# Optimization experiments

Measured on AMD Instinct MI355X. Metric: run time of the kernel, lower is better.

Reference implementation:

```python
import jax, jax.numpy as jnp
import numpy as np

F = 256   # nb_features
H = 8     # nb_heads
B = 4
S = 1024  # q_s == kv_s
SCALE = F ** 0.5  # module MULTIPLIES scores by sqrt(f) when scale=True


def setup_inputs() -> dict:
    key = jax.random.key(0)
    ks = jax.random.split(key, 6)
    return {
        "q_input": jax.random.normal(ks[0], (B, F, S), dtype=jnp.float32),
        "kv_input": jax.random.normal(ks[1], (B, F, S), dtype=jnp.float32),
        "Wq": jax.random.normal(ks[2], (F, F * H), dtype=jnp.float32) * (F ** -0.5),
        "Wk": jax.random.normal(ks[3], (F, F * H), dtype=jnp.float32) * (F ** -0.5),
        "Wv": jax.random.normal(ks[4], (F, F * H), dtype=jnp.float32) * (F ** -0.5),
        "Wz": jax.random.normal(ks[5], (F * H, F), dtype=jnp.float32) * ((F * H) ** -0.5),
    }


def reference(q_input, kv_input, Wq, Wk, Wv, Wz):
    b, f, q_s = q_input.shape
    kv_s = kv_input.shape[2]
    h = H
    # (b, f, s) -> (b, s, f)
    qx = jnp.transpose(q_input, (0, 2, 1))
    kvx = jnp.transpose(kv_input, (0, 2, 1))
    # Linear f -> f*h, then split last dim into (f, h)
    q = (qx @ Wq).reshape(b, q_s, f, h)
    k = (kvx @ Wk).reshape(b, kv_s, f, h)
    v = (kvx @ Wv).reshape(b, kv_s, f, h)
    # sigmoid-gated attention: scores MULTIPLIED by sqrt(f)
    qkt = jnp.einsum('bifh,bjfh->bijh', q, k)
    attn = jax.nn.sigmoid(qkt * SCALE)
    weighted_v = jnp.einsum('bijh,bjfh->bifh', attn, v)  # (b, q_s, f, h)
    z = weighted_v.reshape(b * q_s, f * h)
    out = jax.nn.relu(z @ Wz)  # dropout p=0.0 -> identity
    return jnp.transpose(out.reshape(b, q_s, f), (0, 2, 1))  # (b, f, q_s)
```

## Files before the change

### kernel.cpp

```cpp
#include <hip/hip_runtime.h>
#include <hip/hip_fp16.h>

typedef _Float16 f16;
typedef _Float16 f16x8 __attribute__((ext_vector_type(8)));
typedef float f32x4 __attribute__((ext_vector_type(4)));
typedef unsigned u32x4 __attribute__((ext_vector_type(4)));

#define AS1(p) ((const __attribute__((address_space(1))) void*)(p))
#define AS3(p) ((__attribute__((address_space(3))) void*)(p))

__device__ __forceinline__ void gload16(const void* g, void* l) {
  __builtin_amdgcn_global_load_lds(AS1(g), AS3(l), 16, 0, 0);
}

__device__ __forceinline__ float sgm(float x) {
  return __builtin_amdgcn_rcpf(1.0f + __builtin_amdgcn_exp2f(x * -23.083120654223414f));
}

__device__ __forceinline__ void tbody(const float* __restrict__ ip,
                                      f16* __restrict__ op,
                                      long in_rs, long out_rs) {
  __shared__ float t[64][68];
  int tid = threadIdx.x;
  {
    int c4 = (tid & 15) * 4, r0 = tid >> 4;
#pragma unroll
    for (int p = 0; p < 4; ++p) {
      int r = r0 + 16 * p;
      float4 v = *(const float4*)(ip + (long)r * in_rs + c4);
      t[c4 + 0][r] = v.x; t[c4 + 1][r] = v.y; t[c4 + 2][r] = v.z; t[c4 + 3][r] = v.w;
    }
  }
  __syncthreads();
  {
    int r4 = (tid & 15) * 4, c0 = tid >> 4;
#pragma unroll
    for (int p = 0; p < 4; ++p) {
      int c = c0 + 16 * p;
      float4 v = *(const float4*)(&t[c][r4]);
      union { f16 h[4]; unsigned long long u; } pk;
      pk.h[0] = (f16)v.x; pk.h[1] = (f16)v.y; pk.h[2] = (f16)v.z; pk.h[3] = (f16)v.w;
      *(unsigned long long*)(op + (long)c * out_rs + r4) = pk.u;
    }
  }
}

__global__ __launch_bounds__(256) void tall(
    const float* __restrict__ qin, const float* __restrict__ kvin,
    const float* __restrict__ Wq, const float* __restrict__ Wk,
    const float* __restrict__ Wv, const float* __restrict__ Wz,
    f16* __restrict__ Xq, f16* __restrict__ Xkv,
    f16* __restrict__ Wqt, f16* __restrict__ Wkt, f16* __restrict__ Wvt,
    f16* __restrict__ Wzt) {
  int id = blockIdx.x;
  if (id < 512) {
    int x = id & 15, y = (id >> 4) & 3, z = id >> 6;
    const float* in = (z < 4) ? qin : kvin;
    f16* out = (z < 4) ? Xq : Xkv;
    long b = z & 3;
    tbody(in + b * 262144 + (long)(y * 64) * 1024 + x * 64,
          out + b * 262144 + (long)(x * 64) * 256 + y * 64, 1024, 256);
  } else if (id < 896) {
    int t = id - 512;
    int x = t & 31, y = (t >> 5) & 3, z = t >> 7;
    const float* in = (z == 0) ? Wq : (z == 1) ? Wk : Wv;
    f16* out = (z == 0) ? Wqt : (z == 1) ? Wkt : Wvt;
    tbody(in + (long)(y * 64) * 2048 + x * 64,
          out + (long)(x * 64) * 256 + y * 64, 2048, 256);
  } else {
    int t = id - 896;
    int x = t & 3, y = (t >> 2) & 3;
    long z = t >> 4;
    tbody(Wz + z * 256 + (long)(y * 64) * 2048 + x * 64,
          Wzt + z * 256 + (long)(x * 64) * 2048 + y * 64, 2048, 2048);
  }
}

__global__ __launch_bounds__(256) void projk(
    const f16* __restrict__ Xq, const f16* __restrict__ Xkv,
    const f16* __restrict__ Wqt, const f16* __restrict__ Wkt, const f16* __restrict__ Wvt,
    f16* __restrict__ Qh, f16* __restrict__ Kh, f16* __restrict__ Vt) {
  __shared__ char sm[65536];
  int z = blockIdx.z;
  const f16* A = (z == 0) ? Xq : Xkv;
  const f16* B = (z == 0) ? Wqt : (z == 1) ? Wkt : Wvt;
  int m0 = blockIdx.x * 128, n0 = blockIdx.y * 128;
  int tid = threadIdx.x, wave = tid >> 6, lane = tid & 63;
  int wm = wave & 1, wn = wave >> 1;
  f32x4 acc[4][4];
#pragma unroll
  for (int i = 0; i < 4; ++i)
#pragma unroll
    for (int j = 0; j < 4; ++j) acc[i][j] = (f32x4){0.f, 0.f, 0.f, 0.f};

  auto PSTAGE = [&](int buf, int kt) {
    char* As = sm + buf * 32768;
    char* Bs = As + 16384;
    int k0 = kt * 64;
#pragma unroll
    for (int is = 0; is < 4; ++is) {
      int loff = is * 4096 + wave * 1024;
      int g = loff + lane * 16;
      int row = g >> 7, sl = (g >> 4) & 7;
      int sp = (sl ^ (row & 7)) * 8;
      gload16(A + (long)(m0 + row) * 256 + k0 + sp, As + loff);
      gload16(B + (long)(n0 + row) * 256 + k0 + sp, Bs + loff);
    }
  };

  PSTAGE(0, 0);
  __syncthreads();
  for (int kt = 0; kt < 4; ++kt) {
    int cur = kt & 1;
    if (kt < 3) PSTAGE(cur ^ 1, kt + 1);
    const char* As = sm + cur * 32768;
    const char* Bs = As + 16384;
#pragma unroll
    for (int t = 0; t < 2; ++t) {
      f16x8 af[4], bf[4];
#pragma unroll
      for (int mi = 0; mi < 4; ++mi) {
        int row = wm * 64 + mi * 16 + (lane & 15);
        int sl = (t * 4 + (lane >> 4)) ^ (row & 7);
        af[mi] = *(const f16x8*)(As + row * 128 + sl * 16);
      }
#pragma unroll
      for (int ni = 0; ni < 4; ++ni) {
        int row = wn * 64 + ni * 16 + (lane & 15);
        int sl = (t * 4 + (lane >> 4)) ^ (row & 7);
        bf[ni] = *(const f16x8*)(Bs + row * 128 + sl * 16);
      }
#pragma unroll
      for (int mi = 0; mi < 4; ++mi)
#pragma unroll
        for (int ni = 0; ni < 4; ++ni)
          acc[mi][ni] = __builtin_amdgcn_mfma_f32_16x16x32_f16(af[mi], bf[ni], acc[mi][ni], 0, 0, 0);
    }
    __syncthreads();
  }
#pragma unroll
  for (int mi = 0; mi < 4; ++mi)
#pragma unroll
    for (int ni = 0; ni < 4; ++ni) {
      int cc = wn * 64 + ni * 16 + (lane & 15);
      int rs0 = wm * 64 + mi * 16 + (lane >> 4) * 4;
      union { f16 h[4]; unsigned long long u; } pk;
#pragma unroll
      for (int r = 0; r < 4; ++r) pk.h[r] = (f16)acc[mi][ni][r];
      *(unsigned long long*)(sm + cc * 272 + rs0 * 2) = pk.u;
    }
  __syncthreads();
  if (z < 2) {
    f16* outp = (z == 0) ? Qh : Kh;
#pragma unroll
    for (int pass = 0; pass < 4; ++pass) {
      int item = pass * 256 + tid;
      int rs = item & 127, h = item >> 7;
      int m = m0 + rs, b = m >> 10, s = m & 1023;
      union { unsigned short u16[16]; uint4 q[2]; } pk;
#pragma unroll
      for (int u = 0; u < 16; ++u)
        pk.u16[u] = *(const unsigned short*)(sm + (h + 8 * u) * 272 + rs * 2);
      f16* dst = outp + ((long)(b * 8 + h) * 1024 + s) * 256 + (n0 >> 3);
      *(uint4*)dst = pk.q[0];
      *(uint4*)(dst + 8) = pk.q[1];
    }
  } else {
    int cc = tid >> 1, half = tid & 1;
    int c = n0 + cc, h = c & 7, fi = c >> 3;
    int m = m0 + half * 64;
    int b = m >> 10, s0 = m & 1023;
    uint4 q[8];
#pragma unroll
    for (int j = 0; j < 8; ++j)
      q[j] = *(const uint4*)(sm + cc * 272 + half * 128 + j * 16);
    f16* dst = Vt + ((long)(b * 8 + h) * 256 + fi) * 1024 + s0;
#pragma unroll
    for (int j = 0; j < 8; ++j) *(uint4*)(dst + j * 8) = q[j];
  }
}

__global__ __launch_bounds__(256) void attnk(
    const f16* __restrict__ Qh, const f16* __restrict__ Kh,
    const f16* __restrict__ Vt, f16* __restrict__ Zb) {
  __shared__ char sm[65536];
  int flat = blockIdx.x;
  int xcd = flat & 7, slotb = flat >> 3;
  int bh = xcd + 8 * (slotb & 3);
  int i0 = (slotb >> 2) * 64;
  int tid = threadIdx.x, wave = tid >> 6, lane = tid & 63;
  int l15 = lane & 15, l4 = lane >> 4;
  const f16* Qp = Qh + (long)bh * 262144;
  f16x8 q[8];
  {
    const f16* qr = Qp + (long)(i0 + wave * 16 + l15) * 256 + l4 * 8;
#pragma unroll
    for (int t = 0; t < 8; ++t) q[t] = *(const f16x8*)(qr + t * 32);
  }
  f32x4 acc[16];
#pragma unroll
  for (int n = 0; n < 16; ++n) acc[n] = (f32x4){0.f, 0.f, 0.f, 0.f};

  const char* kp[4];
  const char* vp[4];
  {
    const char* Kb = (const char*)(Kh + (long)bh * 262144);
    const char* Vb = (const char*)(Vt + (long)bh * 262144);
#pragma unroll
    for (int is = 0; is < 4; ++is) {
      int g = is * 4096 + wave * 1024 + lane * 16;
      int krow = g >> 9, ksl = (g >> 4) & 31;
      kp[is] = Kb + krow * 512 + ((ksl ^ krow) * 16);
      int f = g >> 6, jc = (g >> 4) & 3;
      vp[is] = Vb + f * 2048 + ((jc ^ ((f >> 1) & 3)) * 16);
    }
  }
  const int KB  = l15 * 512 + ((l4 * 16) ^ (l15 * 16));
  const int KB2 = KB + 8448;
  const int VB  = 16384 + l15 * 64 + ((l4 ^ ((l15 >> 1) & 3)) * 16);
  const int sdo = wave * 1024;

  auto STAGE = [&](int ob) {
#pragma unroll
    for (int is = 0; is < 4; ++is) {
      gload16(kp[is], sm + ob + is * 4096 + sdo);
      gload16(vp[is], sm + ob + 16384 + is * 4096 + sdo);
      kp[is] += 16384;
      vp[is] += 64;
    }
  };

  STAGE(0);
  __syncthreads();
  int bb = 0;
  for (int jt = 0; jt < 32; ++jt) {
    if (jt < 31) STAGE(bb ^ 32768);
    const int kb = KB ^ bb, kb2 = KB2 ^ bb, vb = VB ^ bb;
    f32x4 s0 = (f32x4){0.f, 0.f, 0.f, 0.f};
    f32x4 s1 = (f32x4){0.f, 0.f, 0.f, 0.f};
    __builtin_amdgcn_s_setprio(1);
#pragma unroll
    for (int t = 0; t < 8; ++t) {
      f16x8 k0 = *(const f16x8*)(sm + (kb ^ (t * 64)));
      f16x8 k1 = *(const f16x8*)(sm + (kb2 ^ (t * 64)));
      s0 = __builtin_amdgcn_mfma_f32_16x16x32_f16(k0, q[t], s0, 0, 0, 0);
      s1 = __builtin_amdgcn_mfma_f32_16x16x32_f16(k1, q[t], s1, 0, 0, 0);
    }
    __builtin_amdgcn_s_setprio(0);
    unsigned u00 = __builtin_bit_cast(unsigned, __builtin_amdgcn_cvt_pkrtz(sgm(s0[0]), sgm(s0[1])));
    unsigned u01 = __builtin_bit_cast(unsigned, __builtin_amdgcn_cvt_pkrtz(sgm(s0[2]), sgm(s0[3])));
    unsigned u10 = __builtin_bit_cast(unsigned, __builtin_amdgcn_cvt_pkrtz(sgm(s1[0]), sgm(s1[1])));
    unsigned u11 = __builtin_bit_cast(unsigned, __builtin_amdgcn_cvt_pkrtz(sgm(s1[2]), sgm(s1[3])));
    auto a0 = __builtin_amdgcn_permlane32_swap(u00, u10, false, false);
    auto w02 = __builtin_amdgcn_permlane16_swap(a0[0], a0[1], false, false);
    auto a1 = __builtin_amdgcn_permlane32_swap(u01, u11, false, false);
    auto w13 = __builtin_amdgcn_permlane16_swap(a1[0], a1[1], false, false);
    u32x4 paw;
    paw[0] = w02[0]; paw[1] = w13[0]; paw[2] = w02[1]; paw[3] = w13[1];
    f16x8 pav = __builtin_bit_cast(f16x8, paw);
    __builtin_amdgcn_s_setprio(1);
#pragma unroll
    for (int n = 0; n < 16; ++n) {
      f16x8 vbf = *(const f16x8*)(sm + (vb ^ (n * 1024)));
      acc[n] = __builtin_amdgcn_mfma_f32_16x16x32_f16(pav, vbf, acc[n], 0, 0, 0);
    }
    __builtin_amdgcn_s_setprio(0);
    __syncthreads();
    bb ^= 32768;
  }
#pragma unroll
  for (int nf = 0; nf < 16; ++nf)
#pragma unroll
    for (int r = 0; r < 4; ++r) {
      int il = wave * 16 + l4 * 4 + r;
      int f = nf * 16 + l15;
      *(f16*)(sm + il * 512 + ((f * 2) ^ (((il >> 2) & 3) << 5))) = (f16)acc[nf][r];
    }
  __syncthreads();
  f16* zp = Zb + ((long)bh * 1024 + i0) * 256;
#pragma unroll
  for (int c = 0; c < 8; ++c) {
    int il = c * 8 + (tid >> 5);
    int fb = (tid & 31) * 16;
    uint4 v = *(const uint4*)(sm + il * 512 + (fb ^ (((il >> 2) & 3) << 5)));
    *(uint4*)((char*)zp + il * 512 + fb) = v;
  }
}

__global__ __launch_bounds__(256) void zkern(
    const f16* __restrict__ Wzt, const f16* __restrict__ Zb,
    float* __restrict__ out) {
  __shared__ char sm[65536];
  int fo0 = blockIdx.x * 64, s0 = blockIdx.y * 64, b = blockIdx.z;
  int tid = threadIdx.x, wave = tid >> 6, lane = tid & 63;
  int wm = wave & 1, wn = wave >> 1;
  f32x4 acc[2][2];
#pragma unroll
  for (int i = 0; i < 2; ++i)
#pragma unroll
    for (int j = 0; j < 2; ++j) acc[i][j] = (f32x4){0.f, 0.f, 0.f, 0.f};

  auto ZSTAGE = [&](int buf, int kt) {
    char* As = sm + buf * 32768;
    char* Bs = As + 16384;
    int k0 = kt * 128, h = k0 >> 8, fi0 = k0 & 255;
#pragma unroll
    for (int is = 0; is < 4; ++is) {
      int loff = is * 4096 + wave * 1024;
      int g = loff + lane * 16;
      int row = g >> 8, sl = (g >> 4) & 15;
      int sp = (sl ^ (row & 15)) * 8;
      gload16(Wzt + (long)(fo0 + row) * 2048 + k0 + sp, As + loff);
      gload16(Zb + ((long)(b * 8 + h) * 1024 + s0 + row) * 256 + fi0 + sp, Bs + loff);
    }
  };

  ZSTAGE(0, 0);
  __syncthreads();
  for (int kt = 0; kt < 16; ++kt) {
    int cur = kt & 1;
    if (kt < 15) ZSTAGE(cur ^ 1, kt + 1);
    const char* As = sm + cur * 32768;
    const char* Bs = As + 16384;
#pragma unroll
    for (int t = 0; t < 4; ++t) {
      f16x8 af[2], bf[2];
#pragma unroll
      for (int mi = 0; mi < 2; ++mi) {
        int row = wm * 32 + mi * 16 + (lane & 15);
        int sl = (t * 4 + (lane >> 4)) ^ (row & 15);
        af[mi] = *(const f16x8*)(As + row * 256 + sl * 16);
      }
#pragma unroll
      for (int ni = 0; ni < 2; ++ni) {
        int row = wn * 32 + ni * 16 + (lane & 15);
        int sl = (t * 4 + (lane >> 4)) ^ (row & 15);
        bf[ni] = *(const f16x8*)(Bs + row * 256 + sl * 16);
      }
#pragma unroll
      for (int mi = 0; mi < 2; ++mi)
#pragma unroll
        for (int ni = 0; ni < 2; ++ni)
          acc[mi][ni] = __builtin_amdgcn_mfma_f32_16x16x32_f16(af[mi], bf[ni], acc[mi][ni], 0, 0, 0);
    }
    __syncthreads();
  }
#pragma unroll
  for (int mi = 0; mi < 2; ++mi)
#pragma unroll
    for (int ni = 0; ni < 2; ++ni)
#pragma unroll
      for (int r = 0; r < 4; ++r) {
        int fo = fo0 + wm * 32 + mi * 16 + (lane >> 4) * 4 + r;
        int s = s0 + wn * 32 + ni * 16 + (lane & 15);
        float v = acc[mi][ni][r];
        out[((long)b * 256 + fo) * 1024 + s] = v > 0.f ? v : 0.f;
      }
}

extern "C" void kernel_launch(void* const* d_in, const int* in_sizes, int n_in,
                              void* d_out, int out_size, void* d_ws, size_t ws_size,
                              hipStream_t stream) {
  const float* qin = (const float*)d_in[0];
  const float* kvin = (const float*)d_in[1];
  const float* Wq = (const float*)d_in[2];
  const float* Wk = (const float*)d_in[3];
  const float* Wv = (const float*)d_in[4];
  const float* Wz = (const float*)d_in[5];
  float* out = (float*)d_out;
  char* ws = (char*)d_ws;
  const long MB = 1 << 20;
  f16* Xq  = (f16*)(ws + 0 * MB);
  f16* Xkv = (f16*)(ws + 2 * MB);
  f16* Wqt = (f16*)(ws + 4 * MB);
  f16* Wkt = (f16*)(ws + 5 * MB);
  f16* Wvt = (f16*)(ws + 6 * MB);
  f16* Wzt = (f16*)(ws + 7 * MB);
  f16* Qh  = (f16*)(ws + 8 * MB);
  f16* Kh  = (f16*)(ws + 24 * MB);
  f16* Vt  = (f16*)(ws + 40 * MB);
  f16* Zb  = Qh;
  dim3 blk(256);
  tall<<<dim3(1024), blk, 0, stream>>>(qin, kvin, Wq, Wk, Wv, Wz,
                                       Xq, Xkv, Wqt, Wkt, Wvt, Wzt);
  projk<<<dim3(32, 16, 3), blk, 0, stream>>>(Xq, Xkv, Wqt, Wkt, Wvt, Qh, Kh, Vt);
  attnk<<<dim3(512), blk, 0, stream>>>(Qh, Kh, Vt, Zb);
  zkern<<<dim3(4, 16, 4), blk, 0, stream>>>(Wzt, Zb, out);
}
```

Before: 113.1 us.

## Switch attention kernel to 32x32x16 MFMA with two 32-row waves per block

The attention kernel moves from 4 waves of 16 query rows using 16x16x32 MFMA to 2 waves of 32 query rows using 32x32x16 MFMA, with a 128-thread block. Each wave now reads K and V tiles from LDS for twice as many rows, which cuts LDS traffic per FLOP, and sigmoid packing uses fewer lane permutes. The LDS-staged coalesced output store is replaced by direct scattered 2-byte global stores. Risks include lower occupancy from fewer waves per block, higher register use (16 q fragments and 8 f32x16 accumulators), and uncoalesced output writes.

```diff
diff --git a/kernel.cpp b/kernel.cpp
--- a/kernel.cpp
+++ b/kernel.cpp
@@ -4,6 +4,7 @@
 typedef _Float16 f16;
 typedef _Float16 f16x8 __attribute__((ext_vector_type(8)));
 typedef float f32x4 __attribute__((ext_vector_type(4)));
+typedef float f32x16 __attribute__((ext_vector_type(16)));
 typedef unsigned u32x4 __attribute__((ext_vector_type(4)));
 
 #define AS1(p) ((const __attribute__((address_space(1))) void*)(p))
@@ -15,6 +16,10 @@
 
 __device__ __forceinline__ float sgm(float x) {
   return __builtin_amdgcn_rcpf(1.0f + __builtin_amdgcn_exp2f(x * -23.083120654223414f));
+}
+
+__device__ __forceinline__ unsigned pk2(float a, float b) {
+  return __builtin_bit_cast(unsigned, __builtin_amdgcn_cvt_pkrtz(a, b));
 }
 
 __device__ __forceinline__ void tbody(const float* __restrict__ ip,
@@ -180,7 +185,7 @@
   }
 }
 
-__global__ __launch_bounds__(256) void attnk(
+__global__ __launch_bounds__(128) void attnk(
     const f16* __restrict__ Qh, const f16* __restrict__ Kh,
     const f16* __restrict__ Vt, f16* __restrict__ Zb) {
   __shared__ char sm[65536];
@@ -189,102 +194,90 @@
   int bh = xcd + 8 * (slotb & 3);
   int i0 = (slotb >> 2) * 64;
   int tid = threadIdx.x, wave = tid >> 6, lane = tid & 63;
-  int l15 = lane & 15, l4 = lane >> 4;
+  int l31 = lane & 31, l5 = lane >> 5;
   const f16* Qp = Qh + (long)bh * 262144;
-  f16x8 q[8];
+  const f16* Kp = Kh + (long)bh * 262144;
+  const f16* Vp = Vt + (long)bh * 262144;
+  int iw = i0 + wave * 32;
+
+  auto STAGE = [&](int ob, int j0) {
+#pragma unroll
+    for (int r = 0; r < 8; ++r) {
+      int o = r * 2048 + tid * 16;
+      {
+        int row = o >> 9, sl = (o >> 4) & 31;
+        gload16(Kp + (long)(j0 + row) * 256 + ((sl ^ row) * 8), sm + ob + o);
+      }
+      {
+        int f = o >> 6, sl = (o >> 4) & 3;
+        int jc = sl ^ ((f >> 1) & 3);
+        gload16(Vp + (long)f * 1024 + j0 + jc * 8, sm + ob + 16384 + o);
+      }
+    }
+  };
+
+  STAGE(0, 0);
+  f16x8 q[16];
   {
-    const f16* qr = Qp + (long)(i0 + wave * 16 + l15) * 256 + l4 * 8;
-#pragma unroll
-    for (int t = 0; t < 8; ++t) q[t] = *(const f16x8*)(qr + t * 32);
-  }
-  f32x4 acc[16];
-#pragma unroll
-  for (int n = 0; n < 16; ++n) acc[n] = (f32x4){0.f, 0.f, 0.f, 0.f};
-
-  const char* kp[4];
-  const char* vp[4];
-  {
-    const char* Kb = (const char*)(Kh + (long)bh * 262144);
-    const char* Vb = (const char*)(Vt + (long)bh * 262144);
-#pragma unroll
-    for (int is = 0; is < 4; ++is) {
-      int g = is * 4096 + wave * 1024 + lane * 16;
-      int krow = g >> 9, ksl = (g >> 4) & 31;
-      kp[is] = Kb + krow * 512 + ((ksl ^ krow) * 16);
-      int f = g >> 6, jc = (g >> 4) & 3;
-      vp[is] = Vb + f * 2048 + ((jc ^ ((f >> 1) & 3)) * 16);
-    }
-  }
-  const int KB  = l15 * 512 + ((l4 * 16) ^ (l15 * 16));
-  const int KB2 = KB + 8448;
-  const int VB  = 16384 + l15 * 64 + ((l4 ^ ((l15 >> 1) & 3)) * 16);
-  const int sdo = wave * 1024;
-
-  auto STAGE = [&](int ob) {
-#pragma unroll
-    for (int is = 0; is < 4; ++is) {
-      gload16(kp[is], sm + ob + is * 4096 + sdo);
-      gload16(vp[is], sm + ob + 16384 + is * 4096 + sdo);
-      kp[is] += 16384;
-      vp[is] += 64;
-    }
-  };
-
-  STAGE(0);
+    const f16* qr = Qp + (long)(iw + l31) * 256 + l5 * 8;
+#pragma unroll
+    for (int t = 0; t < 16; ++t) q[t] = *(const f16x8*)(qr + t * 16);
+  }
+  f32x16 acc[8];
+#pragma unroll
+  for (int n = 0; n < 8; ++n)
+    acc[n] = (f32x16){0.f,0.f,0.f,0.f,0.f,0.f,0.f,0.f,0.f,0.f,0.f,0.f,0.f,0.f,0.f,0.f};
+
+  const int vkey = (l31 >> 1) & 3;
   __syncthreads();
   int bb = 0;
   for (int jt = 0; jt < 32; ++jt) {
-    if (jt < 31) STAGE(bb ^ 32768);
-    const int kb = KB ^ bb, kb2 = KB2 ^ bb, vb = VB ^ bb;
-    f32x4 s0 = (f32x4){0.f, 0.f, 0.f, 0.f};
-    f32x4 s1 = (f32x4){0.f, 0.f, 0.f, 0.f};
+    if (jt < 31) STAGE(bb ^ 32768, (jt + 1) * 32);
+    const char* Ks = sm + bb;
+    const char* Vs = sm + bb + 16384;
+    f32x16 s = (f32x16){0.f,0.f,0.f,0.f,0.f,0.f,0.f,0.f,0.f,0.f,0.f,0.f,0.f,0.f,0.f,0.f};
     __builtin_amdgcn_s_setprio(1);
 #pragma unroll
-    for (int t = 0; t < 8; ++t) {
-      f16x8 k0 = *(const f16x8*)(sm + (kb ^ (t * 64)));
-      f16x8 k1 = *(const f16x8*)(sm + (kb2 ^ (t * 64)));
-      s0 = __builtin_amdgcn_mfma_f32_16x16x32_f16(k0, q[t], s0, 0, 0, 0);
-      s1 = __builtin_amdgcn_mfma_f32_16x16x32_f16(k1, q[t], s1, 0, 0, 0);
+    for (int t = 0; t < 16; ++t) {
+      int c = 2 * t + l5;
+      f16x8 kf = *(const f16x8*)(Ks + l31 * 512 + ((c ^ l31) * 16));
+      s = __builtin_amdgcn_mfma_f32_32x32x16_f16(kf, q[t], s, 0, 0, 0);
     }
     __builtin_amdgcn_s_setprio(0);
-    unsigned u00 = __builtin_bit_cast(unsigned, __builtin_amdgcn_cvt_pkrtz(sgm(s0[0]), sgm(s0[1])));
-    unsigned u01 = __builtin_bit_cast(unsigned, __builtin_amdgcn_cvt_pkrtz(sgm(s0[2]), sgm(s0[3])));
-    unsigned u10 = __builtin_bit_cast(unsigned, __builtin_amdgcn_cvt_pkrtz(sgm(s1[0]), sgm(s1[1])));
-    unsigned u11 = __builtin_bit_cast(unsigned, __builtin_amdgcn_cvt_pkrtz(sgm(s1[2]), sgm(s1[3])));
-    auto a0 = __builtin_amdgcn_permlane32_swap(u00, u10, false, false);
-    auto w02 = __builtin_amdgcn_permlane16_swap(a0[0], a0[1], false, false);
-    auto a1 = __builtin_amdgcn_permlane32_swap(u01, u11, false, false);
-    auto w13 = __builtin_amdgcn_permlane16_swap(a1[0], a1[1], false, false);
-    u32x4 paw;
-    paw[0] = w02[0]; paw[1] = w13[0]; paw[2] = w02[1]; paw[3] = w13[1];
-    f16x8 pav = __builtin_bit_cast(f16x8, paw);
+    unsigned u[8];
+#pragma unroll
+    for (int c2 = 0; c2 < 8; ++c2) u[c2] = pk2(sgm(s[2 * c2]), sgm(s[2 * c2 + 1]));
+    auto w0 = __builtin_amdgcn_permlane32_swap(u[0], u[2], false, false);
+    auto w1 = __builtin_amdgcn_permlane32_swap(u[1], u[3], false, false);
+    auto w2 = __builtin_amdgcn_permlane32_swap(u[4], u[6], false, false);
+    auto w3 = __builtin_amdgcn_permlane32_swap(u[5], u[7], false, false);
+    u32x4 A0w, A1w;
+    A0w[0] = w0[0]; A0w[1] = w1[0]; A0w[2] = w0[1]; A0w[3] = w1[1];
+    A1w[0] = w2[0]; A1w[1] = w3[0]; A1w[2] = w2[1]; A1w[3] = w3[1];
+    f16x8 A0 = __builtin_bit_cast(f16x8, A0w);
+    f16x8 A1 = __builtin_bit_cast(f16x8, A1w);
     __builtin_amdgcn_s_setprio(1);
 #pragma unroll
-    for (int n = 0; n < 16; ++n) {
-      f16x8 vbf = *(const f16x8*)(sm + (vb ^ (n * 1024)));
-      acc[n] = __builtin_amdgcn_mfma_f32_16x16x32_f16(pav, vbf, acc[n], 0, 0, 0);
+    for (int n = 0; n < 8; ++n) {
+      int fb = (n * 32 + l31) * 64;
+      f16x8 v0 = *(const f16x8*)(Vs + fb + ((l5 ^ vkey) * 16));
+      acc[n] = __builtin_amdgcn_mfma_f32_32x32x16_f16(A0, v0, acc[n], 0, 0, 0);
+      f16x8 v1 = *(const f16x8*)(Vs + fb + (((2 + l5) ^ vkey) * 16));
+      acc[n] = __builtin_amdgcn_mfma_f32_32x32x16_f16(A1, v1, acc[n], 0, 0, 0);
     }
     __builtin_amdgcn_s_setprio(0);
     __syncthreads();
     bb ^= 32768;
   }
-#pragma unroll
-  for (int nf = 0; nf < 16; ++nf)
-#pragma unroll
-    for (int r = 0; r < 4; ++r) {
-      int il = wave * 16 + l4 * 4 + r;
-      int f = nf * 16 + l15;
-      *(f16*)(sm + il * 512 + ((f * 2) ^ (((il >> 2) & 3) << 5))) = (f16)acc[nf][r];
-    }
-  __syncthreads();
-  f16* zp = Zb + ((long)bh * 1024 + i0) * 256;
-#pragma unroll
-  for (int c = 0; c < 8; ++c) {
-    int il = c * 8 + (tid >> 5);
-    int fb = (tid & 31) * 16;
-    uint4 v = *(const uint4*)(sm + il * 512 + (fb ^ (((il >> 2) & 3) << 5)));
-    *(uint4*)((char*)zp + il * 512 + fb) = v;
-  }
+  f16* zp = Zb + (long)bh * 262144;
+#pragma unroll
+  for (int n = 0; n < 8; ++n)
+#pragma unroll
+    for (int r = 0; r < 16; ++r) {
+      int i = iw + (r & 3) + 8 * (r >> 2) + 4 * l5;
+      int f = n * 32 + l31;
+      zp[(long)i * 256 + f] = (f16)acc[n][r];
+    }
 }
 
 __global__ __launch_bounds__(256) void zkern(
@@ -384,6 +377,6 @@
   tall<<<dim3(1024), blk, 0, stream>>>(qin, kvin, Wq, Wk, Wv, Wz,
                                        Xq, Xkv, Wqt, Wkt, Wvt, Wzt);
   projk<<<dim3(32, 16, 3), blk, 0, stream>>>(Xq, Xkv, Wqt, Wkt, Wvt, Qh, Kh, Vt);
-  attnk<<<dim3(512), blk, 0, stream>>>(Qh, Kh, Vt, Zb);
+  attnk<<<dim3(512), dim3(128), 0, stream>>>(Qh, Kh, Vt, Zb);
   zkern<<<dim3(4, 16, 4), blk, 0, stream>>>(Wzt, Zb, out);
 }
```

New measurement: 125.9 us. 1.11x slower.

## Load projection GEMM fragments directly from global memory, dropping LDS staging

Applied to the files above, without the earlier changes.

The projection GEMM stops staging A/B tiles through double-buffered LDS with async global-to-LDS loads and per-stage barriers. Each wave now reads its MFMA fragments straight from global memory across the full K=256 loop. This cuts shared memory from 64KB to about 34KB, which may raise occupancy, and removes the main-loop barriers. In exchange, tiles are reloaded redundantly by waves sharing rows or columns, so the kernel leans on L1/L2 bandwidth and the latency of global loads.

```diff
diff --git a/kernel.cpp b/kernel.cpp
--- a/kernel.cpp
+++ b/kernel.cpp
@@ -80,70 +80,49 @@
     const f16* __restrict__ Xq, const f16* __restrict__ Xkv,
     const f16* __restrict__ Wqt, const f16* __restrict__ Wkt, const f16* __restrict__ Wvt,
     f16* __restrict__ Qh, f16* __restrict__ Kh, f16* __restrict__ Vt) {
-  __shared__ char sm[65536];
+  __shared__ char sm[34816];
   int z = blockIdx.z;
   const f16* A = (z == 0) ? Xq : Xkv;
   const f16* B = (z == 0) ? Wqt : (z == 1) ? Wkt : Wvt;
   int m0 = blockIdx.x * 128, n0 = blockIdx.y * 128;
   int tid = threadIdx.x, wave = tid >> 6, lane = tid & 63;
   int wm = wave & 1, wn = wave >> 1;
+  int l15 = lane & 15, l4 = lane >> 4;
   f32x4 acc[4][4];
 #pragma unroll
   for (int i = 0; i < 4; ++i)
 #pragma unroll
     for (int j = 0; j < 4; ++j) acc[i][j] = (f32x4){0.f, 0.f, 0.f, 0.f};
 
-  auto PSTAGE = [&](int buf, int kt) {
-    char* As = sm + buf * 32768;
-    char* Bs = As + 16384;
-    int k0 = kt * 64;
-#pragma unroll
-    for (int is = 0; is < 4; ++is) {
-      int loff = is * 4096 + wave * 1024;
-      int g = loff + lane * 16;
-      int row = g >> 7, sl = (g >> 4) & 7;
-      int sp = (sl ^ (row & 7)) * 8;
-      gload16(A + (long)(m0 + row) * 256 + k0 + sp, As + loff);
-      gload16(B + (long)(n0 + row) * 256 + k0 + sp, Bs + loff);
-    }
-  };
-
-  PSTAGE(0, 0);
-  __syncthreads();
-  for (int kt = 0; kt < 4; ++kt) {
-    int cur = kt & 1;
-    if (kt < 3) PSTAGE(cur ^ 1, kt + 1);
-    const char* As = sm + cur * 32768;
-    const char* Bs = As + 16384;
-#pragma unroll
-    for (int t = 0; t < 2; ++t) {
-      f16x8 af[4], bf[4];
-#pragma unroll
-      for (int mi = 0; mi < 4; ++mi) {
-        int row = wm * 64 + mi * 16 + (lane & 15);
-        int sl = (t * 4 + (lane >> 4)) ^ (row & 7);
-        af[mi] = *(const f16x8*)(As + row * 128 + sl * 16);
-      }
-#pragma unroll
-      for (int ni = 0; ni < 4; ++ni) {
-        int row = wn * 64 + ni * 16 + (lane & 15);
-        int sl = (t * 4 + (lane >> 4)) ^ (row & 7);
-        bf[ni] = *(const f16x8*)(Bs + row * 128 + sl * 16);
-      }
-#pragma unroll
-      for (int mi = 0; mi < 4; ++mi)
-#pragma unroll
-        for (int ni = 0; ni < 4; ++ni)
-          acc[mi][ni] = __builtin_amdgcn_mfma_f32_16x16x32_f16(af[mi], bf[ni], acc[mi][ni], 0, 0, 0);
-    }
-    __syncthreads();
-  }
+  const f16* ar[4];
+  const f16* br[4];
 #pragma unroll
   for (int mi = 0; mi < 4; ++mi)
+    ar[mi] = A + (long)(m0 + wm * 64 + mi * 16 + l15) * 256 + l4 * 8;
+#pragma unroll
+  for (int ni = 0; ni < 4; ++ni)
+    br[ni] = B + (long)(n0 + wn * 64 + ni * 16 + l15) * 256 + l4 * 8;
+
+#pragma unroll
+  for (int tt = 0; tt < 8; ++tt) {
+    f16x8 af[4], bf[4];
+#pragma unroll
+    for (int mi = 0; mi < 4; ++mi) af[mi] = *(const f16x8*)(ar[mi] + tt * 32);
+#pragma unroll
+    for (int ni = 0; ni < 4; ++ni) bf[ni] = *(const f16x8*)(br[ni] + tt * 32);
+#pragma unroll
+    for (int mi = 0; mi < 4; ++mi)
+#pragma unroll
+      for (int ni = 0; ni < 4; ++ni)
+        acc[mi][ni] = __builtin_amdgcn_mfma_f32_16x16x32_f16(af[mi], bf[ni], acc[mi][ni], 0, 0, 0);
+  }
+
+#pragma unroll
+  for (int mi = 0; mi < 4; ++mi)
 #pragma unroll
     for (int ni = 0; ni < 4; ++ni) {
-      int cc = wn * 64 + ni * 16 + (lane & 15);
-      int rs0 = wm * 64 + mi * 16 + (lane >> 4) * 4;
+      int cc = wn * 64 + ni * 16 + l15;
+      int rs0 = wm * 64 + mi * 16 + l4 * 4;
       union { f16 h[4]; unsigned long long u; } pk;
 #pragma unroll
       for (int r = 0; r < 4; ++r) pk.h[r] = (f16)acc[mi][ni][r];
```

New measurement: 131.8 us. 16.6% more time.
